# Kernel tuning notes

Hardware: AMD Instinct MI355X
Metric: run time of the kernel (lower is better)

## Reference

```python
import jax, jax.numpy as jnp
import numpy as np
from math import sqrt

N, L, IN, OUT, H = 100000, 5, 256, 256, 4
DH = OUT // H
RED = OUT // 16  # SE reduction
SCALE = 1.0 / sqrt(OUT)  # note: module scales by 1/sqrt(out_size), not per-head dim


def setup_inputs() -> dict:
    key = jax.random.key(0)
    ks = jax.random.split(key, 12)
    std = 0.02
    return {
        "x": jax.random.normal(ks[0], (N, L, IN), dtype=jnp.float32),
        "Wq": jax.random.normal(ks[1], (H, IN, DH), dtype=jnp.float32) * std,
        "bq": jax.random.normal(ks[2], (H, DH), dtype=jnp.float32) * std,
        "Wk": jax.random.normal(ks[3], (H, IN, DH), dtype=jnp.float32) * std,
        "bk": jax.random.normal(ks[4], (H, DH), dtype=jnp.float32) * std,
        "Wv": jax.random.normal(ks[5], (H, IN, DH), dtype=jnp.float32) * std,
        "bv": jax.random.normal(ks[6], (H, DH), dtype=jnp.float32) * std,
        "W1": jax.random.normal(ks[7], (OUT, RED), dtype=jnp.float32) * std,
        "b1": jax.random.normal(ks[8], (RED,), dtype=jnp.float32) * std,
        "W2": jax.random.normal(ks[9], (RED, OUT), dtype=jnp.float32) * std,
        "b2": jax.random.normal(ks[10], (OUT,), dtype=jnp.float32) * std,
    }


def reference(x, Wq, bq, Wk, bk, Wv, bv, W1, b1, W2, b2):
    # Batched per-head QKV projections: [H, N, L, DH]
    Q = jnp.einsum("nli,hid->hnld", x, Wq) + bq[:, None, None, :]
    K = jnp.einsum("nli,hid->hnld", x, Wk) + bk[:, None, None, :]
    V = jnp.einsum("nli,hid->hnld", x, Wv) + bv[:, None, None, :]
    # attention over the small layer dim L
    attn = jnp.einsum("hnld,hnmd->hnlm", Q, K) * SCALE
    alpha = jax.nn.softmax(attn, axis=-1)  # softmax over dim=2 of [N,L,L] == last axis here
    z = jnp.einsum("hnlm,hnmd->hnld", alpha, V)
    # concat heads -> [N, L, OUT]
    z = jnp.transpose(z, (1, 2, 0, 3)).reshape(N, L, OUT)
    # SE block: squeeze over layer dim, excite with 2-layer MLP gate
    s = z.mean(axis=1, keepdims=True)                      # [N,1,OUT]
    g = jax.nn.sigmoid(jax.nn.relu(s @ W1 + b1) @ W2 + b2)  # [N,1,OUT]
    z = g * z
    return z.mean(axis=1)  # [N, OUT]
```

## Files before the change

### kernel.cpp

```cpp
#include <hip/hip_runtime.h>

typedef unsigned int uint;
typedef unsigned short ushort;

typedef short bfrag __attribute__((ext_vector_type(8)));
typedef float f32x4 __attribute__((ext_vector_type(4)));

__device__ __forceinline__ ushort f2bf(float f) {
  uint u = __float_as_uint(f);
  u = (u + 0x7FFFu + ((u >> 16) & 1u)) >> 16;
  return (ushort)u;
}
__device__ __forceinline__ float bf2f(ushort h) {
  return __uint_as_float(((uint)h) << 16);
}
__device__ __forceinline__ uint cvt_pk_bf16(float lo, float hi) {
  uint r;
  asm("v_cvt_pk_bf16_f32 %0, %1, %2" : "=v"(r) : "v"(lo), "v"(hi));
  return r;
}
__device__ __forceinline__ float sigmoidf(float t) {
  return __builtin_amdgcn_rcpf(1.0f + __expf(-t));
}

__global__ void prep_kernel(const float* __restrict__ Wq, const float* __restrict__ Wk,
                            const float* __restrict__ Wv, const float* __restrict__ W1,
                            ushort* __restrict__ wb, float* __restrict__ w1t) {
  int idx = blockIdx.x * 256 + threadIdx.x;
  if (idx < 196608) {
    int j    = idx & 7;
    int lane = (idx >> 3) & 63;
    int kk   = (idx >> 9) & 7;
    int gnt  = idx >> 12;
    int head = gnt / 12;
    int nh   = (gnt % 12) * 16 + (lane & 15);
    int k    = kk * 32 + (lane >> 4) * 8 + j;
    int sel  = nh >> 6, d = nh & 63;
    const float* W = (sel == 0) ? Wq : ((sel == 1) ? Wk : Wv);
    wb[idx] = f2bf(W[(head * 256 + k) * 64 + d]);
  }
  if (idx < 4096) {
    int j = idx >> 8, c = idx & 255;
    w1t[idx] = W1[c * 16 + j];
  }
}

__global__ __launch_bounds__(256, 2)
void fused_kernel(const float* __restrict__ x,
                  const float* __restrict__ bq, const float* __restrict__ bk,
                  const float* __restrict__ bv,
                  const ushort* __restrict__ wb, const float* __restrict__ w1t,
                  const float* __restrict__ b1, const float* __restrict__ W2,
                  const float* __restrict__ b2, float* __restrict__ out) {
  __shared__ ushort xlds[20480];
  __shared__ ushort qkv[16000];
  __shared__ ushort sbuf[4096];
  __shared__ float  wgt[128];

  const int tid  = threadIdx.x;
  const int lane = tid & 63;
  const int wave = tid >> 6;
  const int ln   = lane & 15;
  const int quad = lane >> 4;
  const int blk  = blockIdx.x;

  {
    const float* xb = x + (size_t)blk * 20480;
#pragma unroll
    for (int it = 0; it < 20; ++it) {
      int f = it * 1024 + tid * 4;
      float4 v = *(const float4*)(xb + f);
      int row = f >> 8;
      int col = f & 255;
      int ch = col >> 3;
      int half = (col >> 2) & 1;
      int phys = ch ^ (row & 7);
      uint2 p;
      p.x = cvt_pk_bf16(v.x, v.y);
      p.y = cvt_pk_bf16(v.z, v.w);
      *(uint2*)(&xlds[row * 256 + phys * 8 + half * 4]) = p;
    }
  }
  __syncthreads();

  const int sample = tid >> 4;
  const int u      = tid & 15;

  const int sl   = ln >> 3;
  const int mm   = ln & 7;
  const int qsel = quad - (sl << 1);
  const bool lo  = (qsel == 0), hi = (qsel == 1);
  const bool lv  = (mm < 5);
  int r0 = (wave * 4 + sl) * 5 + mm;      if (r0 > 79) r0 = 79;
  int r1 = (wave * 4 + 2 + sl) * 5 + mm;  if (r1 > 79) r1 = 79;
  const int bQ0 = r0 * 400 + quad * 16;
  const int bQ1 = r1 * 400 + quad * 16;

  for (int head = 0; head < 4; ++head) {
    f32x4 acc[5][3];
#pragma unroll
    for (int mt = 0; mt < 5; ++mt)
#pragma unroll
      for (int nt = 0; nt < 3; ++nt)
        acc[mt][nt] = (f32x4){0.f, 0.f, 0.f, 0.f};

#pragma unroll
    for (int kk = 0; kk < 8; ++kk) {
      bfrag a[5], b[3];
      int cb = kk * 4 + quad;
#pragma unroll
      for (int mt = 0; mt < 5; ++mt) {
        int row = mt * 16 + ln;
        int off = row * 256 + ((cb ^ (row & 7)) << 3);
        a[mt] = *(const bfrag*)(&xlds[off]);
      }
#pragma unroll
      for (int nt = 0; nt < 3; ++nt) {
        int goff = (((head * 12 + wave * 3 + nt) * 8 + kk) * 64 + lane) * 8;
        b[nt] = *(const bfrag*)(wb + goff);
      }
#pragma unroll
      for (int nt = 0; nt < 3; ++nt)
#pragma unroll
        for (int mt = 0; mt < 5; ++mt)
          acc[mt][nt] = __builtin_amdgcn_mfma_f32_16x16x32_bf16(b[nt], a[mt], acc[mt][nt], 0, 0, 0);
    }

#pragma unroll
    for (int nt = 0; nt < 3; ++nt) {
      int nq = wave * 48 + nt * 16 + quad * 4;
      int sel = nq >> 6, d0 = nq & 63;
      const float* bp = (sel == 0) ? bq : ((sel == 1) ? bk : bv);
      float4 bias = *(const float4*)(bp + head * 64 + d0);
#pragma unroll
      for (int mt = 0; mt < 5; ++mt) {
        int xr = mt * 16 + ln;
        uint2 p;
        p.x = cvt_pk_bf16(acc[mt][nt][0] + bias.x, acc[mt][nt][1] + bias.y);
        p.y = cvt_pk_bf16(acc[mt][nt][2] + bias.z, acc[mt][nt][3] + bias.w);
        *(uint2*)(&qkv[xr * 200 + nq]) = p;
      }
    }
    __syncthreads();

    f32x4 s0 = {0.f, 0.f, 0.f, 0.f}, s1 = {0.f, 0.f, 0.f, 0.f};
    {
      const char* qb = (const char*)qkv;
#pragma unroll
      for (int kk = 0; kk < 2; ++kk) {
        bfrag qf0 = *(const bfrag*)(qb + bQ0 + kk * 64);
        bfrag kf0 = *(const bfrag*)(qb + bQ0 + 128 + kk * 64);
        bfrag qf1 = *(const bfrag*)(qb + bQ1 + kk * 64);
        bfrag kf1 = *(const bfrag*)(qb + bQ1 + 128 + kk * 64);
        s0 = __builtin_amdgcn_mfma_f32_16x16x32_bf16(kf0, qf0, s0, 0, 0, 0);
        s1 = __builtin_amdgcn_mfma_f32_16x16x32_bf16(kf1, qf1, s1, 0, 0, 0);
      }
    }

    auto attn_tile = [&](const f32x4 sS, const int t) {
      float t0 = sS[0] * 0.0625f, t1 = sS[1] * 0.0625f;
      float t2 = sS[2] * 0.0625f, t3 = sS[3] * 0.0625f;
      float pm = lo ? fmaxf(fmaxf(t0, t1), fmaxf(t2, t3)) : (hi ? t0 : -1e30f);
      pm = fmaxf(pm, __shfl_xor(pm, 16));
      pm = fmaxf(pm, __shfl_xor(pm, 32));
      float e0 = __expf(t0 - pm), e1 = __expf(t1 - pm);
      float e2 = __expf(t2 - pm), e3 = __expf(t3 - pm);
      float ps = lo ? (e0 + e1 + e2 + e3) : (hi ? e0 : 0.f);
      ps += __shfl_xor(ps, 16);
      ps += __shfl_xor(ps, 32);
      float inv = 0.2f * __builtin_amdgcn_rcpf(ps);
      float c0 = ((lo || hi) && lv) ? e0 * inv : 0.f;
      float c1 = (lo && lv) ? e1 * inv : 0.f;
      float c2 = (lo && lv) ? e2 * inv : 0.f;
      float c3 = (lo && lv) ? e3 * inv : 0.f;
      c0 += __shfl_xor(c0, 1); c0 += __shfl_xor(c0, 2); c0 += __shfl_xor(c0, 4);
      c1 += __shfl_xor(c1, 1); c1 += __shfl_xor(c1, 2); c1 += __shfl_xor(c1, 4);
      c2 += __shfl_xor(c2, 1); c2 += __shfl_xor(c2, 2); c2 += __shfl_xor(c2, 4);
      c3 += __shfl_xor(c3, 1); c3 += __shfl_xor(c3, 2); c3 += __shfl_xor(c3, 4);
      int smp = wave * 4 + t * 2 + sl;
      if (mm == 0) {
        if (qsel == 0) {
          *(float4*)(wgt + smp * 8) = make_float4(c0, c1, c2, c3);
        } else if (qsel == 1) {
          wgt[smp * 8 + 4] = c0;
        }
      }
    };
    attn_tile(s0, 0);
    attn_tile(s1, 1);
    __builtin_amdgcn_wave_barrier();

    {
      float4 w03 = *(const float4*)(wgt + sample * 8);
      float w4 = wgt[sample * 8 + 4];
      float a0 = 0.f, a1 = 0.f, a2 = 0.f, a3 = 0.f;
#pragma unroll
      for (int m = 0; m < 5; ++m) {
        float wv = (m == 0) ? w03.x : (m == 1) ? w03.y : (m == 2) ? w03.z
                 : (m == 3) ? w03.w : w4;
        uint2 v = *(const uint2*)(&qkv[(sample * 5 + m) * 200 + 128 + u * 4]);
        a0 += wv * bf2f((ushort)(v.x & 0xffff));
        a1 += wv * bf2f((ushort)(v.x >> 16));
        a2 += wv * bf2f((ushort)(v.y & 0xffff));
        a3 += wv * bf2f((ushort)(v.y >> 16));
      }
      uint2 p;
      p.x = cvt_pk_bf16(a0, a1);
      p.y = cvt_pk_bf16(a2, a3);
      *(uint2*)(&sbuf[sample * 256 + head * 64 + u * 4]) = p;
    }
    __syncthreads();
  }

  float rse;
  {
    float accv = b1[u];
    const float* wr = w1t + u * 256;
#pragma unroll 4
    for (int c = 0; c < 256; c += 4) {
      uint2 sv = *(const uint2*)(&sbuf[sample * 256 + c]);
      float4 wv = *(const float4*)(wr + c);
      accv += bf2f((ushort)(sv.x & 0xffff)) * wv.x + bf2f((ushort)(sv.x >> 16)) * wv.y
            + bf2f((ushort)(sv.y & 0xffff)) * wv.z + bf2f((ushort)(sv.y >> 16)) * wv.w;
    }
    rse = fmaxf(accv, 0.f);
  }

  {
    float g[16];
#pragma unroll
    for (int i = 0; i < 16; ++i) g[i] = b2[u * 16 + i];
    const int lbase = tid & 48;
#pragma unroll
    for (int j = 0; j < 16; ++j) {
      float rj = __shfl(rse, lbase | j, 64);
      const float* w2r = W2 + j * 256 + u * 16;
#pragma unroll
      for (int i = 0; i < 16; i += 4) {
        float4 wv = *(const float4*)(w2r + i);
        g[i + 0] += rj * wv.x; g[i + 1] += rj * wv.y;
        g[i + 2] += rj * wv.z; g[i + 3] += rj * wv.w;
      }
    }
    float* ob = out + ((size_t)blk * 16 + sample) * 256 + u * 16;
#pragma unroll
    for (int i = 0; i < 16; i += 4) {
      int c = u * 16 + i;
      uint2 sv = *(const uint2*)(&sbuf[sample * 256 + c]);
      float4 ov;
      ov.x = sigmoidf(g[i + 0]) * bf2f((ushort)(sv.x & 0xffff));
      ov.y = sigmoidf(g[i + 1]) * bf2f((ushort)(sv.x >> 16));
      ov.z = sigmoidf(g[i + 2]) * bf2f((ushort)(sv.y & 0xffff));
      ov.w = sigmoidf(g[i + 3]) * bf2f((ushort)(sv.y >> 16));
      *(float4*)(ob + i) = ov;
    }
  }
}

extern "C" void kernel_launch(void* const* d_in, const int* in_sizes, int n_in,
                              void* d_out, int out_size, void* d_ws, size_t ws_size,
                              hipStream_t stream) {
  const float* x  = (const float*)d_in[0];
  const float* Wq = (const float*)d_in[1];
  const float* bq = (const float*)d_in[2];
  const float* Wk = (const float*)d_in[3];
  const float* bk = (const float*)d_in[4];
  const float* Wv = (const float*)d_in[5];
  const float* bv = (const float*)d_in[6];
  const float* W1 = (const float*)d_in[7];
  const float* b1 = (const float*)d_in[8];
  const float* W2 = (const float*)d_in[9];
  const float* b2 = (const float*)d_in[10];

  ushort* wb  = (ushort*)d_ws;
  float*  w1t = (float*)((char*)d_ws + 393216);

  prep_kernel<<<768, 256, 0, stream>>>(Wq, Wk, Wv, W1, wb, w1t);
  fused_kernel<<<6250, 256, 0, stream>>>(x, bq, bk, bv, wb, w1t, b1, W2, b2,
                                         (float*)d_out);
}
```

Before: 1.169 ms.

## Prefetch QKV weights into registers, run SE MLP on MFMA, use DPP reductions

Each head's projection weight fragments are now preloaded into registers, and the next head's are loaded while the current head's attention runs, so the GEMM no longer waits on global loads. Both SE gate layers now use bf16 MFMA, with a hi/lo split of weights and activations to keep near-fp32 accuracy; prep stores the W1 and W2 fragments in that form. Two of the three shuffle reductions in the softmax weighting become DPP adds. The cost is much higher register pressure (48 bfrag registers live) at launch_bounds(256,2), which could cause spills or lower occupancy.

```diff
diff --git a/kernel.cpp b/kernel.cpp
--- a/kernel.cpp
+++ b/kernel.cpp
@@ -22,10 +22,17 @@
 __device__ __forceinline__ float sigmoidf(float t) {
   return __builtin_amdgcn_rcpf(1.0f + __expf(-t));
 }
+template <int CTRL>
+__device__ __forceinline__ float dppadd(float v) {
+  int r = __builtin_amdgcn_update_dpp(0, __float_as_int(v), CTRL, 0xf, 0xf, true);
+  return v + __int_as_float(r);
+}
 
 __global__ void prep_kernel(const float* __restrict__ Wq, const float* __restrict__ Wk,
                             const float* __restrict__ Wv, const float* __restrict__ W1,
-                            ushort* __restrict__ wb, float* __restrict__ w1t) {
+                            const float* __restrict__ W2,
+                            ushort* __restrict__ wb, ushort* __restrict__ w1b,
+                            ushort* __restrict__ w2b) {
   int idx = blockIdx.x * 256 + threadIdx.x;
   if (idx < 196608) {
     int j    = idx & 7;
@@ -40,8 +47,25 @@
     wb[idx] = f2bf(W[(head * 256 + k) * 64 + d]);
   }
   if (idx < 4096) {
-    int j = idx >> 8, c = idx & 255;
-    w1t[idx] = W1[c * 16 + j];
+    int jj   = idx & 7;
+    int lane = (idx >> 3) & 63;
+    int kk   = idx >> 9;
+    int c    = kk * 32 + (lane >> 4) * 8 + jj;
+    float v  = W1[c * 16 + (lane & 15)];
+    ushort h = f2bf(v);
+    w1b[idx] = h;
+    w1b[4096 + idx] = f2bf(v - bf2f(h));
+  }
+  if (idx < 8192) {
+    int jj   = idx & 7;
+    int lane = (idx >> 3) & 63;
+    int nt   = idx >> 9;
+    int quad = lane >> 4;
+    int k    = (quad & 1) * 8 + jj;
+    float v  = (quad < 2) ? W2[k * 256 + nt * 16 + (lane & 15)] : 0.f;
+    ushort h = f2bf(v);
+    w2b[idx] = h;
+    w2b[8192 + idx] = f2bf(v - bf2f(h));
   }
 }
 
@@ -49,9 +73,10 @@
 void fused_kernel(const float* __restrict__ x,
                   const float* __restrict__ bq, const float* __restrict__ bk,
                   const float* __restrict__ bv,
-                  const ushort* __restrict__ wb, const float* __restrict__ w1t,
-                  const float* __restrict__ b1, const float* __restrict__ W2,
-                  const float* __restrict__ b2, float* __restrict__ out) {
+                  const ushort* __restrict__ wb, const ushort* __restrict__ w1b,
+                  const ushort* __restrict__ w2b,
+                  const float* __restrict__ b1, const float* __restrict__ b2,
+                  float* __restrict__ out) {
   __shared__ ushort xlds[20480];
   __shared__ ushort qkv[16000];
   __shared__ ushort sbuf[4096];
@@ -81,6 +106,15 @@
       *(uint2*)(&xlds[row * 256 + phys * 8 + half * 4]) = p;
     }
   }
+
+  const bfrag* wfr = (const bfrag*)wb;
+  bfrag Wc[24];
+#pragma unroll
+  for (int kk = 0; kk < 8; ++kk)
+#pragma unroll
+    for (int nt = 0; nt < 3; ++nt)
+      Wc[kk * 3 + nt] = wfr[((wave * 3 + nt) * 8 + kk) * 64 + lane];
+
   __syncthreads();
 
   const int sample = tid >> 4;
@@ -96,6 +130,7 @@
   const int bQ0 = r0 * 400 + quad * 16;
   const int bQ1 = r1 * 400 + quad * 16;
 
+#pragma unroll 1
   for (int head = 0; head < 4; ++head) {
     f32x4 acc[5][3];
 #pragma unroll
@@ -106,7 +141,7 @@
 
 #pragma unroll
     for (int kk = 0; kk < 8; ++kk) {
-      bfrag a[5], b[3];
+      bfrag a[5];
       int cb = kk * 4 + quad;
 #pragma unroll
       for (int mt = 0; mt < 5; ++mt) {
@@ -115,15 +150,19 @@
         a[mt] = *(const bfrag*)(&xlds[off]);
       }
 #pragma unroll
-      for (int nt = 0; nt < 3; ++nt) {
-        int goff = (((head * 12 + wave * 3 + nt) * 8 + kk) * 64 + lane) * 8;
-        b[nt] = *(const bfrag*)(wb + goff);
-      }
-#pragma unroll
       for (int nt = 0; nt < 3; ++nt)
 #pragma unroll
         for (int mt = 0; mt < 5; ++mt)
-          acc[mt][nt] = __builtin_amdgcn_mfma_f32_16x16x32_bf16(b[nt], a[mt], acc[mt][nt], 0, 0, 0);
+          acc[mt][nt] = __builtin_amdgcn_mfma_f32_16x16x32_bf16(Wc[kk * 3 + nt], a[mt], acc[mt][nt], 0, 0, 0);
+    }
+
+    bfrag Wn[24];
+    if (head < 3) {
+#pragma unroll
+      for (int kk = 0; kk < 8; ++kk)
+#pragma unroll
+        for (int nt = 0; nt < 3; ++nt)
+          Wn[kk * 3 + nt] = wfr[(((head + 1) * 12 + wave * 3 + nt) * 8 + kk) * 64 + lane];
     }
 
 #pragma unroll
@@ -173,10 +212,10 @@
       float c1 = (lo && lv) ? e1 * inv : 0.f;
       float c2 = (lo && lv) ? e2 * inv : 0.f;
       float c3 = (lo && lv) ? e3 * inv : 0.f;
-      c0 += __shfl_xor(c0, 1); c0 += __shfl_xor(c0, 2); c0 += __shfl_xor(c0, 4);
-      c1 += __shfl_xor(c1, 1); c1 += __shfl_xor(c1, 2); c1 += __shfl_xor(c1, 4);
-      c2 += __shfl_xor(c2, 1); c2 += __shfl_xor(c2, 2); c2 += __shfl_xor(c2, 4);
-      c3 += __shfl_xor(c3, 1); c3 += __shfl_xor(c3, 2); c3 += __shfl_xor(c3, 4);
+      c0 = dppadd<0xB1>(c0); c0 = dppadd<0x4E>(c0); c0 += __shfl_xor(c0, 4);
+      c1 = dppadd<0xB1>(c1); c1 = dppadd<0x4E>(c1); c1 += __shfl_xor(c1, 4);
+      c2 = dppadd<0xB1>(c2); c2 = dppadd<0x4E>(c2); c2 += __shfl_xor(c2, 4);
+      c3 = dppadd<0xB1>(c3); c3 = dppadd<0x4E>(c3); c3 += __shfl_xor(c3, 4);
       int smp = wave * 4 + t * 2 + sl;
       if (mm == 0) {
         if (qsel == 0) {
@@ -210,50 +249,67 @@
       *(uint2*)(&sbuf[sample * 256 + head * 64 + u * 4]) = p;
     }
     __syncthreads();
-  }
-
-  float rse;
+
+    if (head < 3) {
+#pragma unroll
+      for (int i = 0; i < 24; ++i) Wc[i] = Wn[i];
+    }
+  }
+
+  const bfrag* w1f = (const bfrag*)w1b;
+  f32x4 racc;
   {
-    float accv = b1[u];
-    const float* wr = w1t + u * 256;
-#pragma unroll 4
-    for (int c = 0; c < 256; c += 4) {
-      uint2 sv = *(const uint2*)(&sbuf[sample * 256 + c]);
-      float4 wv = *(const float4*)(wr + c);
-      accv += bf2f((ushort)(sv.x & 0xffff)) * wv.x + bf2f((ushort)(sv.x >> 16)) * wv.y
-            + bf2f((ushort)(sv.y & 0xffff)) * wv.z + bf2f((ushort)(sv.y >> 16)) * wv.w;
-    }
-    rse = fmaxf(accv, 0.f);
-  }
-
+    float4 b1v = *(const float4*)(b1 + quad * 4);
+    racc[0] = b1v.x; racc[1] = b1v.y; racc[2] = b1v.z; racc[3] = b1v.w;
+#pragma unroll
+    for (int kk = 0; kk < 8; ++kk) {
+      bfrag sB = *(const bfrag*)(&sbuf[ln * 256 + kk * 32 + quad * 8]);
+      racc = __builtin_amdgcn_mfma_f32_16x16x32_bf16(w1f[kk * 64 + lane], sB, racc, 0, 0, 0);
+      racc = __builtin_amdgcn_mfma_f32_16x16x32_bf16(w1f[512 + kk * 64 + lane], sB, racc, 0, 0, 0);
+    }
+#pragma unroll
+    for (int r = 0; r < 4; ++r) racc[r] = fmaxf(racc[r], 0.f);
+  }
+  ushort* rb = qkv;
   {
-    float g[16];
-#pragma unroll
-    for (int i = 0; i < 16; ++i) g[i] = b2[u * 16 + i];
-    const int lbase = tid & 48;
-#pragma unroll
-    for (int j = 0; j < 16; ++j) {
-      float rj = __shfl(rse, lbase | j, 64);
-      const float* w2r = W2 + j * 256 + u * 16;
-#pragma unroll
-      for (int i = 0; i < 16; i += 4) {
-        float4 wv = *(const float4*)(w2r + i);
-        g[i + 0] += rj * wv.x; g[i + 1] += rj * wv.y;
-        g[i + 2] += rj * wv.z; g[i + 3] += rj * wv.w;
-      }
-    }
-    float* ob = out + ((size_t)blk * 16 + sample) * 256 + u * 16;
-#pragma unroll
-    for (int i = 0; i < 16; i += 4) {
-      int c = u * 16 + i;
-      uint2 sv = *(const uint2*)(&sbuf[sample * 256 + c]);
-      float4 ov;
-      ov.x = sigmoidf(g[i + 0]) * bf2f((ushort)(sv.x & 0xffff));
-      ov.y = sigmoidf(g[i + 1]) * bf2f((ushort)(sv.x >> 16));
-      ov.z = sigmoidf(g[i + 2]) * bf2f((ushort)(sv.y & 0xffff));
-      ov.w = sigmoidf(g[i + 3]) * bf2f((ushort)(sv.y >> 16));
-      *(float4*)(ob + i) = ov;
-    }
+    uint hx = cvt_pk_bf16(racc[0], racc[1]);
+    uint hy = cvt_pk_bf16(racc[2], racc[3]);
+    float l0 = racc[0] - __uint_as_float(hx << 16);
+    float l1 = racc[1] - __uint_as_float(hx & 0xffff0000u);
+    float l2 = racc[2] - __uint_as_float(hy << 16);
+    float l3 = racc[3] - __uint_as_float(hy & 0xffff0000u);
+    uint2 hp; hp.x = hx; hp.y = hy;
+    uint2 lp; lp.x = cvt_pk_bf16(l0, l1); lp.y = cvt_pk_bf16(l2, l3);
+    *(uint2*)(&rb[ln * 24 + quad * 4]) = hp;
+    *(uint2*)(&rb[384 + ln * 24 + quad * 4]) = lp;
+  }
+
+  const bfrag* w2f = (const bfrag*)w2b;
+  bfrag rH = {0, 0, 0, 0, 0, 0, 0, 0}, rL = {0, 0, 0, 0, 0, 0, 0, 0};
+  if (quad < 2) {
+    rH = *(const bfrag*)(&rb[ln * 24 + quad * 8]);
+    rL = *(const bfrag*)(&rb[384 + ln * 24 + quad * 8]);
+  }
+  float* ob = out + ((size_t)blk * 16 + ln) * 256;
+#pragma unroll
+  for (int t = 0; t < 4; ++t) {
+    int nt = wave * 4 + t;
+    float4 b2v = *(const float4*)(b2 + nt * 16 + quad * 4);
+    f32x4 g;
+    g[0] = b2v.x; g[1] = b2v.y; g[2] = b2v.z; g[3] = b2v.w;
+    bfrag wh = w2f[nt * 64 + lane];
+    bfrag wl = w2f[1024 + nt * 64 + lane];
+    g = __builtin_amdgcn_mfma_f32_16x16x32_bf16(wh, rH, g, 0, 0, 0);
+    g = __builtin_amdgcn_mfma_f32_16x16x32_bf16(wh, rL, g, 0, 0, 0);
+    g = __builtin_amdgcn_mfma_f32_16x16x32_bf16(wl, rH, g, 0, 0, 0);
+    int c = nt * 16 + quad * 4;
+    uint2 sv = *(const uint2*)(&sbuf[ln * 256 + c]);
+    float4 ov;
+    ov.x = sigmoidf(g[0]) * bf2f((ushort)(sv.x & 0xffff));
+    ov.y = sigmoidf(g[1]) * bf2f((ushort)(sv.x >> 16));
+    ov.z = sigmoidf(g[2]) * bf2f((ushort)(sv.y & 0xffff));
+    ov.w = sigmoidf(g[3]) * bf2f((ushort)(sv.y >> 16));
+    *(float4*)(ob + c) = ov;
   }
 }
 
@@ -273,9 +329,10 @@
   const float* b2 = (const float*)d_in[10];
 
   ushort* wb  = (ushort*)d_ws;
-  float*  w1t = (float*)((char*)d_ws + 393216);
-
-  prep_kernel<<<768, 256, 0, stream>>>(Wq, Wk, Wv, W1, wb, w1t);
-  fused_kernel<<<6250, 256, 0, stream>>>(x, bq, bk, bv, wb, w1t, b1, W2, b2,
+  ushort* w1b = (ushort*)((char*)d_ws + 393216);
+  ushort* w2b = (ushort*)((char*)d_ws + 409600);
+
+  prep_kernel<<<768, 256, 0, stream>>>(Wq, Wk, Wv, W1, W2, wb, w1b, w2b);
+  fused_kernel<<<6250, 256, 0, stream>>>(x, bq, bk, bv, wb, w1b, w2b, b1, b2,
                                          (float*)d_out);
 }
```

Result: slower. 1.296 ms (+10.9%).
